# Performance work log

Hardware: AMD Instinct MI355X
Metric: run time of the kernel (lower is better)

The kernel has to match this reference:

```python
import jax, jax.numpy as jnp
import numpy as np

NEG_INF = -1e9
LEAKY_SLOPE = 0.2


def setup_inputs() -> dict:
    key = jax.random.key(0)
    k1, k2, k3, k4, k5 = jax.random.split(key, 5)
    B, N, F_in, F_out = 8, 2048, 256, 256
    x = jax.random.normal(k1, (B, N, F_in), dtype=jnp.float32)
    adj = jax.random.randint(k2, (B, N, N), 0, 2, dtype=jnp.int32)
    W = jax.random.normal(k3, (F_out, F_in), dtype=jnp.float32) * 0.05
    a_src = jax.random.normal(k4, (F_out,), dtype=jnp.float32) * 0.05
    a_dst = jax.random.normal(k5, (F_out,), dtype=jnp.float32) * 0.05
    return {"x": x, "adj": adj, "W": W, "a_src": a_src, "a_dst": a_dst}


def reference(x, adj, W, a_src, a_dst):
    # h: (B, N, F_out)
    h = jnp.einsum("bnf,of->bno", x, W)
    # a([h_i ; h_j]) == h_i @ a_src + h_j @ a_dst  (avoids O(N^2, 2F) concat)
    s_src = h @ a_src  # (B, N) score contribution of row node i
    s_dst = h @ a_dst  # (B, N) score contribution of col node j
    e = s_src[:, :, None] + s_dst[:, None, :]  # (B, N, N)
    e = jax.nn.leaky_relu(e, negative_slope=LEAKY_SLOPE)
    e = jnp.where(adj == 0, jnp.float32(NEG_INF), e)
    alpha = jax.nn.softmax(e, axis=-1)  # dropout is identity in eval mode
    h_prime = jnp.einsum("bij,bjo->bio", alpha, h)
    return h_prime
```

## Files before the change

### kernel.cpp

```cpp
#include <hip/hip_runtime.h>
#include <hip/hip_bf16.h>
#include <cstdint>
#include <cstddef>

typedef __attribute__((ext_vector_type(8))) short short8;
typedef __attribute__((ext_vector_type(4))) short short4v;
typedef __attribute__((ext_vector_type(4))) float floatx4;
typedef __attribute__((ext_vector_type(16))) float floatx16;
typedef unsigned short ushort_t;

#define LOG2E 1.44269504088896340736f

__device__ __forceinline__ unsigned short f2bf(float f) {
    unsigned u = __float_as_uint(f);
    u += 0x7FFFu + ((u >> 16) & 1u);
    return (unsigned short)(u >> 16);
}
__device__ __forceinline__ float bf2f(unsigned short s) {
    return __uint_as_float(((unsigned)s) << 16);
}

__global__ __launch_bounds__(256) void wprep(const float* __restrict__ W,
                                             ushort_t* __restrict__ Wb) {
    int t = blockIdx.x * 256 + threadIdx.x;
    float4 v = ((const float4*)W)[t];
    short4v s;
    s[0] = (short)f2bf(v.x); s[1] = (short)f2bf(v.y);
    s[2] = (short)f2bf(v.z); s[3] = (short)f2bf(v.w);
    ((short4v*)Wb)[t] = s;
}

__global__ __launch_bounds__(1024) void gemm_h(const float* __restrict__ x,
                                               const ushort_t* __restrict__ Wb,
                                               ushort_t* __restrict__ hT,
                                               const float* __restrict__ a_src,
                                               const float* __restrict__ a_dst,
                                               float* __restrict__ s_src,
                                               float* __restrict__ s_dst) {
    const int tid = threadIdx.x;
    const int w = tid >> 6, lane = tid & 63;
    const int q = lane >> 4, t16 = lane & 15;
    const int jg = w >> 2, og = w & 3;

    __shared__ ushort_t wt[256][72];
    __shared__ float sred[2][4][64];

    const int jrow = blockIdx.x * 64 + jg * 16 + t16;
    const float* xr = x + (size_t)jrow * 256 + q * 8;
    short8 af[8];
#pragma unroll
    for (int kb = 0; kb < 8; ++kb) {
        float4 v0 = *(const float4*)(xr + kb * 32);
        float4 v1 = *(const float4*)(xr + kb * 32 + 4);
        short8 a;
        a[0] = (short)f2bf(v0.x); a[1] = (short)f2bf(v0.y);
        a[2] = (short)f2bf(v0.z); a[3] = (short)f2bf(v0.w);
        a[4] = (short)f2bf(v1.x); a[5] = (short)f2bf(v1.y);
        a[6] = (short)f2bf(v1.z); a[7] = (short)f2bf(v1.w);
        af[kb] = a;
    }

    floatx4 acc[4] = {};
#pragma unroll
    for (int kp = 0; kp < 4; ++kp) {
        if (kp) __syncthreads();
#pragma unroll
        for (int r = 0; r < 2; ++r) {
            int G = tid + 1024 * r;
            int row = G >> 3, g = G & 7;
            int4 wv = *(const int4*)(Wb + (size_t)row * 256 + kp * 64 + g * 8);
            *(int4*)(&wt[row][g * 8]) = wv;
        }
        __syncthreads();
#pragma unroll
        for (int ks = 0; ks < 2; ++ks) {
#pragma unroll
            for (int ct = 0; ct < 4; ++ct) {
                short8 bf = *(const short8*)(&wt[og * 64 + ct * 16 + t16][ks * 32 + q * 8]);
                acc[ct] = __builtin_amdgcn_mfma_f32_16x16x32_bf16(af[kp * 2 + ks], bf, acc[ct], 0, 0, 0);
            }
        }
    }

    const int jbase = blockIdx.x * 64 + jg * 16 + q * 4;
    const int b = jbase >> 11, jj = jbase & 2047;
#pragma unroll
    for (int ct = 0; ct < 4; ++ct) {
        const int o = og * 64 + ct * 16 + t16;
        short4v sv;
        sv[0] = (short)f2bf(acc[ct][0]);
        sv[1] = (short)f2bf(acc[ct][1]);
        sv[2] = (short)f2bf(acc[ct][2]);
        sv[3] = (short)f2bf(acc[ct][3]);
        *(short4v*)(hT + ((size_t)b * 256 + o) * 2048 + jj) = sv;
    }

    float psv[4] = {}, pdv[4] = {};
#pragma unroll
    for (int ct = 0; ct < 4; ++ct) {
        const int o = og * 64 + ct * 16 + t16;
        float as = a_src[o], ad = a_dst[o];
#pragma unroll
        for (int r = 0; r < 4; ++r) {
            psv[r] = __fmaf_rn(acc[ct][r], as, psv[r]);
            pdv[r] = __fmaf_rn(acc[ct][r], ad, pdv[r]);
        }
    }
#pragma unroll
    for (int m = 1; m < 16; m <<= 1) {
#pragma unroll
        for (int r = 0; r < 4; ++r) {
            psv[r] += __shfl_xor(psv[r], m);
            pdv[r] += __shfl_xor(pdv[r], m);
        }
    }
    if (t16 == 0) {
#pragma unroll
        for (int r = 0; r < 4; ++r) {
            sred[0][og][jg * 16 + q * 4 + r] = psv[r];
            sred[1][og][jg * 16 + q * 4 + r] = pdv[r];
        }
    }
    __syncthreads();
    if (tid < 64) {
        float ss = sred[0][0][tid] + sred[0][1][tid] + sred[0][2][tid] + sred[0][3][tid];
        float dd = sred[1][0][tid] + sred[1][1][tid] + sred[1][2][tid] + sred[1][3][tid];
        s_src[blockIdx.x * 64 + tid] = ss;
        s_dst[blockIdx.x * 64 + tid] = dd;
    }
}

__global__ __launch_bounds__(1024) void attn(const ushort_t* __restrict__ hT,
                                             const int* __restrict__ adj,
                                             const float* __restrict__ s_src,
                                             const float* __restrict__ s_dst,
                                             float* __restrict__ out) {
    const int tid = threadIdx.x;
    const int w = tid >> 6;
    const int lane = tid & 63;
    const int l5 = lane & 31, hi = lane >> 5;
    const int b = blockIdx.x;
    const int i0 = blockIdx.y * 64;

    __shared__ ushort_t hts[2][256][40];
    __shared__ ushort_t ps[2][64][40];
    __shared__ float sdl[2048];
    __shared__ float rls[64];

    const float* sdb = s_dst + (size_t)b * 2048;
    {
        int idx = tid * 2;
        float2 v = *(const float2*)(sdb + idx);
        v.x *= LOG2E; v.y *= LOG2E;
        *(float2*)(&sdl[idx]) = v;
    }

    const int ip = w * 4 + (lane >> 4);
    const int jp = lane & 15;
    const float si = s_src[(size_t)b * 2048 + i0 + ip] * LOG2E;
    const int* adjr = adj + ((size_t)b * 2048 + i0 + ip) * 2048 + jp * 2;

    const int hrow = tid >> 2, hseg = tid & 3;
    const ushort_t* hTg = hT + ((size_t)b * 256 + hrow) * 2048 + hseg * 8;

    const int osub = (w & 7) * 32, ih = (w >> 3) * 32;

    floatx16 acc = {};
    float lsum = 0.f;
    int4 hreg;
    int2 a2;

    hreg = *(const int4*)(hTg);
    a2 = *(const int2*)(adjr);
    __syncthreads();

    for (int c = 0; c < 64; ++c) {
        const int buf = c & 1;
        *(int4*)(&hts[buf][hrow][hseg * 8]) = hreg;
        int2 ac = a2;
        if (c < 63) {
            hreg = *(const int4*)(hTg + (c + 1) * 32);
            a2 = *(const int2*)(adjr + (size_t)(c + 1) * 32);
        }
        {
            float2 sd = *(const float2*)(&sdl[c * 32 + jp * 2]);
            float t0 = si + sd.x;
            float t1 = si + sd.y;
            float l0 = fmaxf(t0, 0.2f * t0);
            float l1 = fmaxf(t1, 0.2f * t1);
            float p0 = __builtin_amdgcn_exp2f(l0);
            float p1 = __builtin_amdgcn_exp2f(l1);
            p0 = (ac.x != 0) ? p0 : 0.0f;
            p1 = (ac.y != 0) ? p1 : 0.0f;
            unsigned short u0 = f2bf(p0);
            unsigned short u1 = f2bf(p1);
            lsum += bf2f(u0) + bf2f(u1);
            *(unsigned*)(&ps[buf][ip][jp * 2]) = (unsigned)u0 | ((unsigned)u1 << 16);
        }
        __syncthreads();
#pragma unroll
        for (int ks = 0; ks < 2; ++ks) {
            short8 afr = *(const short8*)(&hts[buf][osub + l5][ks * 16 + hi * 8]);
            short8 bfr = *(const short8*)(&ps[buf][ih + l5][ks * 16 + hi * 8]);
            acc = __builtin_amdgcn_mfma_f32_32x32x16_bf16(afr, bfr, acc, 0, 0, 0);
        }
    }

#pragma unroll
    for (int m = 1; m < 16; m <<= 1) lsum += __shfl_xor(lsum, m);
    if (jp == 0) rls[ip] = lsum;
    __syncthreads();

    {
        const int i = ih + l5;
        const float s = rls[i];
        const float rl = (s > 0.f) ? 1.0f / s : 0.0f;
        float* orow = out + ((size_t)b * 2048 + i0 + i) * 256 + osub;
#pragma unroll
        for (int rq = 0; rq < 4; ++rq) {
            floatx4 v;
            v[0] = acc[rq * 4 + 0] * rl;
            v[1] = acc[rq * 4 + 1] * rl;
            v[2] = acc[rq * 4 + 2] * rl;
            v[3] = acc[rq * 4 + 3] * rl;
            *(floatx4*)(orow + rq * 8 + hi * 4) = v;
        }
    }
}

extern "C" void kernel_launch(void* const* d_in, const int* in_sizes, int n_in,
                              void* d_out, int out_size, void* d_ws, size_t ws_size,
                              hipStream_t stream) {
    const float* x     = (const float*)d_in[0];
    const int*   adj   = (const int*)d_in[1];
    const float* W     = (const float*)d_in[2];
    const float* a_src = (const float*)d_in[3];
    const float* a_dst = (const float*)d_in[4];
    float* out = (float*)d_out;

    char* ws = (char*)d_ws;
    ushort_t* hT = (ushort_t*)ws;
    float* s_src = (float*)(ws + (size_t)8 * 1024 * 1024);
    float* s_dst = s_src + 16384;
    ushort_t* Wb = (ushort_t*)(s_dst + 16384);

    wprep<<<64, 256, 0, stream>>>(W, Wb);
    gemm_h<<<256, 1024, 0, stream>>>(x, Wb, hT, a_src, a_dst, s_src, s_dst);
    attn<<<dim3(8, 32), 1024, 0, stream>>>(hT, adj, s_src, s_dst, out);
}
```

Baseline: 249.0 us.

## Load hT MFMA fragments directly to registers and widen attention chunks

Measured after the change: 273.2 us. +9.7%, slower.

```diff
diff --git a/kernel.cpp b/kernel.cpp
--- a/kernel.cpp
+++ b/kernel.cpp
@@ -20,18 +20,8 @@
     return __uint_as_float(((unsigned)s) << 16);
 }
 
-__global__ __launch_bounds__(256) void wprep(const float* __restrict__ W,
-                                             ushort_t* __restrict__ Wb) {
-    int t = blockIdx.x * 256 + threadIdx.x;
-    float4 v = ((const float4*)W)[t];
-    short4v s;
-    s[0] = (short)f2bf(v.x); s[1] = (short)f2bf(v.y);
-    s[2] = (short)f2bf(v.z); s[3] = (short)f2bf(v.w);
-    ((short4v*)Wb)[t] = s;
-}
-
 __global__ __launch_bounds__(1024) void gemm_h(const float* __restrict__ x,
-                                               const ushort_t* __restrict__ Wb,
+                                               const float* __restrict__ W,
                                                ushort_t* __restrict__ hT,
                                                const float* __restrict__ a_src,
                                                const float* __restrict__ a_dst,
@@ -68,8 +58,15 @@
         for (int r = 0; r < 2; ++r) {
             int G = tid + 1024 * r;
             int row = G >> 3, g = G & 7;
-            int4 wv = *(const int4*)(Wb + (size_t)row * 256 + kp * 64 + g * 8);
-            *(int4*)(&wt[row][g * 8]) = wv;
+            const float* wsrc = W + (size_t)row * 256 + kp * 64 + g * 8;
+            float4 f0 = *(const float4*)(wsrc);
+            float4 f1 = *(const float4*)(wsrc + 4);
+            short8 wv;
+            wv[0] = (short)f2bf(f0.x); wv[1] = (short)f2bf(f0.y);
+            wv[2] = (short)f2bf(f0.z); wv[3] = (short)f2bf(f0.w);
+            wv[4] = (short)f2bf(f1.x); wv[5] = (short)f2bf(f1.y);
+            wv[6] = (short)f2bf(f1.z); wv[7] = (short)f2bf(f1.w);
+            *(short8*)(&wt[row][g * 8]) = wv;
         }
         __syncthreads();
 #pragma unroll
@@ -142,8 +139,7 @@
     const int b = blockIdx.x;
     const int i0 = blockIdx.y * 64;
 
-    __shared__ ushort_t hts[2][256][40];
-    __shared__ ushort_t ps[2][64][40];
+    __shared__ ushort_t ps[2][64][72];
     __shared__ float sdl[2048];
     __shared__ float rls[64];
 
@@ -155,60 +151,96 @@
         *(float2*)(&sdl[idx]) = v;
     }
 
-    const int ip = w * 4 + (lane >> 4);
-    const int jp = lane & 15;
+    const int ip = tid >> 4, jq = tid & 15;
     const float si = s_src[(size_t)b * 2048 + i0 + ip] * LOG2E;
-    const int* adjr = adj + ((size_t)b * 2048 + i0 + ip) * 2048 + jp * 2;
-
-    const int hrow = tid >> 2, hseg = tid & 3;
-    const ushort_t* hTg = hT + ((size_t)b * 256 + hrow) * 2048 + hseg * 8;
+    const int* adjr = adj + ((size_t)b * 2048 + i0 + ip) * 2048 + jq * 4;
 
     const int osub = (w & 7) * 32, ih = (w >> 3) * 32;
+    const ushort_t* hTg = hT + ((size_t)b * 256 + osub + l5) * 2048 + hi * 8;
 
     floatx16 acc = {};
     float lsum = 0.f;
-    int4 hreg;
-    int2 a2;
-
-    hreg = *(const int4*)(hTg);
-    a2 = *(const int2*)(adjr);
+    int4 aE, aO;
+    short8 af0[4], af1[4];
+
+    aE = *(const int4*)(adjr);
+    aO = *(const int4*)(adjr + 64);
+#pragma unroll
+    for (int ks = 0; ks < 4; ++ks)
+        af0[ks] = *(const short8*)(hTg + ks * 16);
     __syncthreads();
 
-    for (int c = 0; c < 64; ++c) {
-        const int buf = c & 1;
-        *(int4*)(&hts[buf][hrow][hseg * 8]) = hreg;
-        int2 ac = a2;
-        if (c < 63) {
-            hreg = *(const int4*)(hTg + (c + 1) * 32);
-            a2 = *(const int2*)(adjr + (size_t)(c + 1) * 32);
-        }
-        {
-            float2 sd = *(const float2*)(&sdl[c * 32 + jp * 2]);
-            float t0 = si + sd.x;
-            float t1 = si + sd.y;
-            float l0 = fmaxf(t0, 0.2f * t0);
-            float l1 = fmaxf(t1, 0.2f * t1);
-            float p0 = __builtin_amdgcn_exp2f(l0);
-            float p1 = __builtin_amdgcn_exp2f(l1);
-            p0 = (ac.x != 0) ? p0 : 0.0f;
-            p1 = (ac.y != 0) ? p1 : 0.0f;
-            unsigned short u0 = f2bf(p0);
-            unsigned short u1 = f2bf(p1);
-            lsum += bf2f(u0) + bf2f(u1);
-            *(unsigned*)(&ps[buf][ip][jp * 2]) = (unsigned)u0 | ((unsigned)u1 << 16);
-        }
+#pragma unroll 1
+    for (int it = 0; it < 16; ++it) {
+        const int sc = it * 2;
+        {
+            float4 sd = *(const float4*)(&sdl[sc * 64 + jq * 4]);
+            float sv[4] = {sd.x, sd.y, sd.z, sd.w};
+            int mv[4] = {aE.x, aE.y, aE.z, aE.w};
+            short4v pv;
+#pragma unroll
+            for (int e = 0; e < 4; ++e) {
+                float t = si + sv[e];
+                float lr = fmaxf(t, 0.2f * t);
+                float pe = __builtin_amdgcn_exp2f(lr);
+                pe = (mv[e] != 0) ? pe : 0.0f;
+                unsigned short u = f2bf(pe);
+                lsum += bf2f(u);
+                pv[e] = (short)u;
+            }
+            *(short4v*)(&ps[0][ip][jq * 4]) = pv;
+        }
+        {
+            const int nc = (sc + 2 < 32) ? sc + 2 : 31;
+            aE = *(const int4*)(adjr + (size_t)nc * 64);
+        }
+#pragma unroll
+        for (int ks = 0; ks < 4; ++ks)
+            af1[ks] = *(const short8*)(hTg + (size_t)(sc + 1) * 64 + ks * 16);
         __syncthreads();
 #pragma unroll
-        for (int ks = 0; ks < 2; ++ks) {
-            short8 afr = *(const short8*)(&hts[buf][osub + l5][ks * 16 + hi * 8]);
-            short8 bfr = *(const short8*)(&ps[buf][ih + l5][ks * 16 + hi * 8]);
-            acc = __builtin_amdgcn_mfma_f32_32x32x16_bf16(afr, bfr, acc, 0, 0, 0);
+        for (int ks = 0; ks < 4; ++ks) {
+            short8 bfr = *(const short8*)(&ps[0][ih + l5][ks * 16 + hi * 8]);
+            acc = __builtin_amdgcn_mfma_f32_32x32x16_bf16(af0[ks], bfr, acc, 0, 0, 0);
+        }
+        {
+            float4 sd = *(const float4*)(&sdl[(sc + 1) * 64 + jq * 4]);
+            float sv[4] = {sd.x, sd.y, sd.z, sd.w};
+            int mv[4] = {aO.x, aO.y, aO.z, aO.w};
+            short4v pv;
+#pragma unroll
+            for (int e = 0; e < 4; ++e) {
+                float t = si + sv[e];
+                float lr = fmaxf(t, 0.2f * t);
+                float pe = __builtin_amdgcn_exp2f(lr);
+                pe = (mv[e] != 0) ? pe : 0.0f;
+                unsigned short u = f2bf(pe);
+                lsum += bf2f(u);
+                pv[e] = (short)u;
+            }
+            *(short4v*)(&ps[1][ip][jq * 4]) = pv;
+        }
+        {
+            const int nc = (sc + 3 < 32) ? sc + 3 : 31;
+            aO = *(const int4*)(adjr + (size_t)nc * 64);
+        }
+        {
+            const int na = (sc + 2 < 32) ? sc + 2 : 31;
+#pragma unroll
+            for (int ks = 0; ks < 4; ++ks)
+                af0[ks] = *(const short8*)(hTg + (size_t)na * 64 + ks * 16);
+        }
+        __syncthreads();
+#pragma unroll
+        for (int ks = 0; ks < 4; ++ks) {
+            short8 bfr = *(const short8*)(&ps[1][ih + l5][ks * 16 + hi * 8]);
+            acc = __builtin_amdgcn_mfma_f32_32x32x16_bf16(af1[ks], bfr, acc, 0, 0, 0);
         }
     }
 
 #pragma unroll
     for (int m = 1; m < 16; m <<= 1) lsum += __shfl_xor(lsum, m);
-    if (jp == 0) rls[ip] = lsum;
+    if (jq == 0) rls[ip] = lsum;
     __syncthreads();
 
     {
@@ -242,9 +274,7 @@
     ushort_t* hT = (ushort_t*)ws;
     float* s_src = (float*)(ws + (size_t)8 * 1024 * 1024);
     float* s_dst = s_src + 16384;
-    ushort_t* Wb = (ushort_t*)(s_dst + 16384);
-
-    wprep<<<64, 256, 0, stream>>>(W, Wb);
-    gemm_h<<<256, 1024, 0, stream>>>(x, Wb, hT, a_src, a_dst, s_src, s_dst);
+
+    gemm_h<<<256, 1024, 0, stream>>>(x, W, hT, a_src, a_dst, s_src, s_dst);
     attn<<<dim3(8, 32), 1024, 0, stream>>>(hT, adj, s_src, s_dst, out);
 }
```

## Pack adjacency into bitmask in projection kernel and fuse W conversion

Applied to the files above, without the earlier changes.

After: 298.8 us. 20.0% more time.

```diff
diff --git a/kernel.cpp b/kernel.cpp
--- a/kernel.cpp
+++ b/kernel.cpp
@@ -8,6 +8,7 @@
 typedef __attribute__((ext_vector_type(4))) float floatx4;
 typedef __attribute__((ext_vector_type(16))) float floatx16;
 typedef unsigned short ushort_t;
+typedef unsigned long long u64_t;
 
 #define LOG2E 1.44269504088896340736f
 
@@ -20,23 +21,15 @@
     return __uint_as_float(((unsigned)s) << 16);
 }
 
-__global__ __launch_bounds__(256) void wprep(const float* __restrict__ W,
-                                             ushort_t* __restrict__ Wb) {
-    int t = blockIdx.x * 256 + threadIdx.x;
-    float4 v = ((const float4*)W)[t];
-    short4v s;
-    s[0] = (short)f2bf(v.x); s[1] = (short)f2bf(v.y);
-    s[2] = (short)f2bf(v.z); s[3] = (short)f2bf(v.w);
-    ((short4v*)Wb)[t] = s;
-}
-
 __global__ __launch_bounds__(1024) void gemm_h(const float* __restrict__ x,
-                                               const ushort_t* __restrict__ Wb,
+                                               const float* __restrict__ W,
+                                               const int* __restrict__ adj,
                                                ushort_t* __restrict__ hT,
                                                const float* __restrict__ a_src,
                                                const float* __restrict__ a_dst,
                                                float* __restrict__ s_src,
-                                               float* __restrict__ s_dst) {
+                                               float* __restrict__ s_dst,
+                                               u64_t* __restrict__ adjb) {
     const int tid = threadIdx.x;
     const int w = tid >> 6, lane = tid & 63;
     const int q = lane >> 4, t16 = lane & 15;
@@ -68,8 +61,15 @@
         for (int r = 0; r < 2; ++r) {
             int G = tid + 1024 * r;
             int row = G >> 3, g = G & 7;
-            int4 wv = *(const int4*)(Wb + (size_t)row * 256 + kp * 64 + g * 8);
-            *(int4*)(&wt[row][g * 8]) = wv;
+            const float* wsrc = W + (size_t)row * 256 + kp * 64 + g * 8;
+            float4 f0 = *(const float4*)(wsrc);
+            float4 f1 = *(const float4*)(wsrc + 4);
+            short8 wv;
+            wv[0] = (short)f2bf(f0.x); wv[1] = (short)f2bf(f0.y);
+            wv[2] = (short)f2bf(f0.z); wv[3] = (short)f2bf(f0.w);
+            wv[4] = (short)f2bf(f1.x); wv[5] = (short)f2bf(f1.y);
+            wv[6] = (short)f2bf(f1.z); wv[7] = (short)f2bf(f1.w);
+            *(short8*)(&wt[row][g * 8]) = wv;
         }
         __syncthreads();
 #pragma unroll
@@ -128,10 +128,24 @@
         s_src[blockIdx.x * 64 + tid] = ss;
         s_dst[blockIdx.x * 64 + tid] = dd;
     }
+
+    {
+        const int row0 = blockIdx.x * 64 + w * 4;
+#pragma unroll
+        for (int rr = 0; rr < 4; ++rr) {
+            const int* ap = adj + (size_t)(row0 + rr) * 2048 + lane;
+            u64_t* bp = adjb + (size_t)(row0 + rr) * 32;
+#pragma unroll 4
+            for (int g = 0; g < 32; ++g) {
+                u64_t mk = __ballot(ap[g * 64] != 0);
+                if (lane == 0) bp[g] = mk;
+            }
+        }
+    }
 }
 
 __global__ __launch_bounds__(1024) void attn(const ushort_t* __restrict__ hT,
-                                             const int* __restrict__ adj,
+                                             const u64_t* __restrict__ adjb,
                                              const float* __restrict__ s_src,
                                              const float* __restrict__ s_dst,
                                              float* __restrict__ out) {
@@ -158,7 +172,7 @@
     const int ip = w * 4 + (lane >> 4);
     const int jp = lane & 15;
     const float si = s_src[(size_t)b * 2048 + i0 + ip] * LOG2E;
-    const int* adjr = adj + ((size_t)b * 2048 + i0 + ip) * 2048 + jp * 2;
+    const uint2* amr = (const uint2*)(adjb + ((size_t)b * 2048 + i0 + ip) * 32);
 
     const int hrow = tid >> 2, hseg = tid & 3;
     const ushort_t* hTg = hT + ((size_t)b * 256 + hrow) * 2048 + hseg * 8;
@@ -168,42 +182,72 @@
     floatx16 acc = {};
     float lsum = 0.f;
     int4 hreg;
-    int2 a2;
+    uint2 amc, amcN;
 
     hreg = *(const int4*)(hTg);
-    a2 = *(const int2*)(adjr);
+    amc = amr[0];
     __syncthreads();
 
-    for (int c = 0; c < 64; ++c) {
-        const int buf = c & 1;
-        *(int4*)(&hts[buf][hrow][hseg * 8]) = hreg;
-        int2 ac = a2;
-        if (c < 63) {
-            hreg = *(const int4*)(hTg + (c + 1) * 32);
-            a2 = *(const int2*)(adjr + (size_t)(c + 1) * 32);
-        }
+#pragma unroll 1
+    for (int it = 0; it < 32; ++it) {
+        const int c = it * 2;
+        *(int4*)(&hts[0][hrow][hseg * 8]) = hreg;
+        hreg = *(const int4*)(hTg + (size_t)(c + 1) * 32);
+        amcN = amr[(it + 1 < 32) ? it + 1 : 31];
         {
             float2 sd = *(const float2*)(&sdl[c * 32 + jp * 2]);
+            unsigned m0 = (amc.x >> (jp * 2)) & 1u;
+            unsigned m1 = (amc.x >> (jp * 2 + 1)) & 1u;
             float t0 = si + sd.x;
             float t1 = si + sd.y;
             float l0 = fmaxf(t0, 0.2f * t0);
             float l1 = fmaxf(t1, 0.2f * t1);
             float p0 = __builtin_amdgcn_exp2f(l0);
             float p1 = __builtin_amdgcn_exp2f(l1);
-            p0 = (ac.x != 0) ? p0 : 0.0f;
-            p1 = (ac.y != 0) ? p1 : 0.0f;
+            p0 = m0 ? p0 : 0.0f;
+            p1 = m1 ? p1 : 0.0f;
             unsigned short u0 = f2bf(p0);
             unsigned short u1 = f2bf(p1);
             lsum += bf2f(u0) + bf2f(u1);
-            *(unsigned*)(&ps[buf][ip][jp * 2]) = (unsigned)u0 | ((unsigned)u1 << 16);
+            *(unsigned*)(&ps[0][ip][jp * 2]) = (unsigned)u0 | ((unsigned)u1 << 16);
         }
         __syncthreads();
 #pragma unroll
         for (int ks = 0; ks < 2; ++ks) {
-            short8 afr = *(const short8*)(&hts[buf][osub + l5][ks * 16 + hi * 8]);
-            short8 bfr = *(const short8*)(&ps[buf][ih + l5][ks * 16 + hi * 8]);
+            short8 afr = *(const short8*)(&hts[0][osub + l5][ks * 16 + hi * 8]);
+            short8 bfr = *(const short8*)(&ps[0][ih + l5][ks * 16 + hi * 8]);
             acc = __builtin_amdgcn_mfma_f32_32x32x16_bf16(afr, bfr, acc, 0, 0, 0);
         }
+        *(int4*)(&hts[1][hrow][hseg * 8]) = hreg;
+        {
+            const int nh = (c + 2 < 64) ? c + 2 : 63;
+            hreg = *(const int4*)(hTg + (size_t)nh * 32);
+        }
+        {
+            float2 sd = *(const float2*)(&sdl[(c + 1) * 32 + jp * 2]);
+            unsigned m0 = (amc.y >> (jp * 2)) & 1u;
+            unsigned m1 = (amc.y >> (jp * 2 + 1)) & 1u;
+            float t0 = si + sd.x;
+            float t1 = si + sd.y;
+            float l0 = fmaxf(t0, 0.2f * t0);
+            float l1 = fmaxf(t1, 0.2f * t1);
+            float p0 = __builtin_amdgcn_exp2f(l0);
+            float p1 = __builtin_amdgcn_exp2f(l1);
+            p0 = m0 ? p0 : 0.0f;
+            p1 = m1 ? p1 : 0.0f;
+            unsigned short u0 = f2bf(p0);
+            unsigned short u1 = f2bf(p1);
+            lsum += bf2f(u0) + bf2f(u1);
+            *(unsigned*)(&ps[1][ip][jp * 2]) = (unsigned)u0 | ((unsigned)u1 << 16);
+        }
+        __syncthreads();
+#pragma unroll
+        for (int ks = 0; ks < 2; ++ks) {
+            short8 afr = *(const short8*)(&hts[1][osub + l5][ks * 16 + hi * 8]);
+            short8 bfr = *(const short8*)(&ps[1][ih + l5][ks * 16 + hi * 8]);
+            acc = __builtin_amdgcn_mfma_f32_32x32x16_bf16(afr, bfr, acc, 0, 0, 0);
+        }
+        amc = amcN;
     }
 
 #pragma unroll
@@ -242,9 +286,8 @@
     ushort_t* hT = (ushort_t*)ws;
     float* s_src = (float*)(ws + (size_t)8 * 1024 * 1024);
     float* s_dst = s_src + 16384;
-    ushort_t* Wb = (ushort_t*)(s_dst + 16384);
-
-    wprep<<<64, 256, 0, stream>>>(W, Wb);
-    gemm_h<<<256, 1024, 0, stream>>>(x, Wb, hT, a_src, a_dst, s_src, s_dst);
-    attn<<<dim3(8, 32), 1024, 0, stream>>>(hT, adj, s_src, s_dst, out);
-}
+    u64_t* adjb  = (u64_t*)(s_dst + 16384);
+
+    gemm_h<<<256, 1024, 0, stream>>>(x, W, adj, hT, a_src, a_dst, s_src, s_dst, adjb);
+    attn<<<dim3(8, 32), 1024, 0, stream>>>(hT, adjb, s_src, s_dst, out);
+}
```
